# Optimization experiments

Measured on AMD Instinct MI355X. Metric: run time of the kernel, lower is better.

The kernel has to match this reference:

```python
import jax, jax.numpy as jnp
import numpy as np

N = 100000
E = 600000
H = 128
OUT = 64
L = 3

def glorot(key, shape):
    fan_in, fan_out = shape[0], shape[1]
    lim = jnp.sqrt(6.0 / (fan_in + fan_out))
    return jax.random.uniform(key, shape, jnp.float32, -lim, lim)

def setup_inputs() -> dict:
    key = jax.random.key(0)
    ks = jax.random.split(key, 20)
    x = jax.random.normal(ks[0], (N, H), jnp.float32)
    edge_index = jax.random.randint(ks[1], (2, E), 0, N, jnp.int64)
    edge_attr = jax.random.uniform(ks[2], (E, 1), jnp.float32)
    # stacked per-layer params [L, ...]
    W_lin = jnp.stack([glorot(jax.random.fold_in(ks[3], i), (H, H)) for i in range(L)])
    b_lin = jnp.zeros((L, H), jnp.float32)
    W_msg = jnp.stack([glorot(jax.random.fold_in(ks[4], i), (H + 1, H)) for i in range(L)])
    b_msg = jnp.zeros((L, H), jnp.float32)
    W_l = jnp.stack([glorot(jax.random.fold_in(ks[5], i), (H, H)) for i in range(L)])
    b_l = jnp.zeros((L, H), jnp.float32)
    W_r = jnp.stack([glorot(jax.random.fold_in(ks[6], i), (H, H)) for i in range(L)])
    W_dec = glorot(ks[7], (H, H))
    b_dec = jnp.zeros((H,), jnp.float32)
    W_fin = glorot(ks[8], (H, OUT))
    b_fin = jnp.zeros((OUT,), jnp.float32)
    return {"x": x, "edge_attr": edge_attr, "W_lin": W_lin, "b_lin": b_lin,
            "W_msg": W_msg, "b_msg": b_msg, "W_l": W_l, "b_l": b_l, "W_r": W_r,
            "W_dec": W_dec, "b_dec": b_dec, "W_fin": W_fin, "b_fin": b_fin,
            "edge_index": edge_index}

def reference(x, edge_attr, W_lin, b_lin, W_msg, b_msg, W_l, b_l, W_r,
              W_dec, b_dec, W_fin, b_fin, edge_index):
    src, dst = edge_index[0], edge_index[1]  # j -> i (source_to_target)
    # mean-aggregation denominator: in-degree clamped to 1
    deg = jax.ops.segment_sum(jnp.ones((E,), jnp.float32), dst, num_segments=N)
    inv_deg = (1.0 / jnp.maximum(deg, 1.0))[:, None]  # [N,1]
    for l in range(L):
        h = jax.nn.relu(x @ W_lin[l] + b_lin[l])          # [N,H]
        msg_in = jnp.concatenate([h[src], edge_attr], -1)  # [E,H+1]
        msg = jax.nn.relu(msg_in @ W_msg[l] + b_msg[l])    # [E,H]
        agg = jax.ops.segment_sum(msg, dst, num_segments=N) * inv_deg  # [N,H]
        out = (agg @ W_l[l] + b_l[l]) + x @ W_r[l]         # lin_l(agg) + lin_r(x_r)
        x = jax.nn.relu(out)  # dropout p=0.0 -> identity
    emb = jax.nn.relu(x @ W_dec + b_dec)
    logits = emb @ W_fin + b_fin  # [N,OUT]
    return logits
```

## Files before the change

### kernel.cpp

```cpp
#include <hip/hip_runtime.h>

using short8 = __attribute__((ext_vector_type(8))) short;
using f32x4  = __attribute__((ext_vector_type(4))) float;

constexpr int HD = 128;

__device__ __forceinline__ unsigned short f2bf(float f) {
    unsigned u = __builtin_bit_cast(unsigned, f);
    u += 0x7fffu + ((u >> 16) & 1u);
    return (unsigned short)(u >> 16);
}
__device__ __forceinline__ float bflo(unsigned u) { return __builtin_bit_cast(float, u << 16); }
__device__ __forceinline__ float bfhi(unsigned u) { return __builtin_bit_cast(float, u & 0xffff0000u); }

__device__ __forceinline__ short8 ldg8(const unsigned short* p) {
    return *reinterpret_cast<const short8*>(p);
}

template<bool DUAL, bool CHAIN, int NC2, bool F32OUT>
__global__ __launch_bounds__(256)
void k_gemm_s(const unsigned short* __restrict__ A1, const unsigned short* __restrict__ Wt1,
              const unsigned short* __restrict__ A2, const unsigned short* __restrict__ Wt2,
              const unsigned short* __restrict__ Wtc, const float* __restrict__ b1,
              const float* __restrict__ b2, void* __restrict__ Out, int nrows)
{
    __shared__ __align__(16) unsigned short As1[64 * HD];
    __shared__ __align__(16) unsigned short As2[DUAL ? 64 * HD : 8];
    __shared__ __align__(16) unsigned short Hs [CHAIN ? 64 * HD : 8];

    const int tid  = threadIdx.x;
    const int lane = tid & 63, wave = tid >> 6;
    const int lr = lane & 15, lg = lane >> 4;
    const int row0 = blockIdx.x * 64;

#pragma unroll
    for (int it = 0; it < 4; ++it) {
        const int q   = wave * 4 + it;
        const int c   = q * 64 + lane;
        const int row = c >> 4, cw = c & 15;
        int grow = row0 + row; grow = grow < nrows ? grow : nrows - 1;
        const int gco = (cw ^ (row & 7)) << 3;
        __builtin_amdgcn_global_load_lds((const unsigned int*)(A1 + (long)grow * HD + gco),
                                         (unsigned int*)&As1[q * 512], 16, 0, 0);
        if constexpr (DUAL)
            __builtin_amdgcn_global_load_lds((const unsigned int*)(A2 + (long)grow * HD + gco),
                                             (unsigned int*)&As2[q * 512], 16, 0, 0);
    }

    const int cb1 = wave * 32;
    short8 bf1[2][4];
#pragma unroll
    for (int ct = 0; ct < 2; ++ct) {
        const unsigned short* bp = Wt1 + (long)(cb1 + ct * 16 + lr) * HD + lg * 8;
#pragma unroll
        for (int kt = 0; kt < 4; ++kt) bf1[ct][kt] = ldg8(bp + kt * 32);
    }
    short8 bf2[DUAL ? 2 : 1][4];
    if constexpr (DUAL) {
#pragma unroll
        for (int ct = 0; ct < 2; ++ct) {
            const unsigned short* bp = Wt2 + (long)(cb1 + ct * 16 + lr) * HD + lg * 8;
#pragma unroll
            for (int kt = 0; kt < 4; ++kt) bf2[ct][kt] = ldg8(bp + kt * 32);
        }
    }
    constexpr int CT2 = CHAIN ? (NC2 / 64) : 1;
    const int cb2 = wave * (NC2 / 4);
    short8 bfc[CT2][4];
    if constexpr (CHAIN) {
#pragma unroll
        for (int ct = 0; ct < CT2; ++ct) {
            const unsigned short* bp = Wtc + (long)(cb2 + ct * 16 + lr) * HD + lg * 8;
#pragma unroll
            for (int kt = 0; kt < 4; ++kt) bfc[ct][kt] = ldg8(bp + kt * 32);
        }
    }

    __syncthreads();

    f32x4 acc[4][2] = {};
#pragma unroll
    for (int kt = 0; kt < 4; ++kt) {
        short8 af[4];
#pragma unroll
        for (int rt = 0; rt < 4; ++rt)
            af[rt] = *reinterpret_cast<const short8*>(
                &As1[(rt * 16 + lr) * HD + (((kt * 4 + lg) ^ (lr & 7)) << 3)]);
#pragma unroll
        for (int rt = 0; rt < 4; ++rt)
#pragma unroll
            for (int ct = 0; ct < 2; ++ct)
                acc[rt][ct] = __builtin_amdgcn_mfma_f32_16x16x32_bf16(af[rt], bf1[ct][kt], acc[rt][ct], 0, 0, 0);
        if constexpr (DUAL) {
            short8 af2[4];
#pragma unroll
            for (int rt = 0; rt < 4; ++rt)
                af2[rt] = *reinterpret_cast<const short8*>(
                    &As2[(rt * 16 + lr) * HD + (((kt * 4 + lg) ^ (lr & 7)) << 3)]);
#pragma unroll
            for (int rt = 0; rt < 4; ++rt)
#pragma unroll
                for (int ct = 0; ct < 2; ++ct)
                    acc[rt][ct] = __builtin_amdgcn_mfma_f32_16x16x32_bf16(af2[rt], bf2[ct][kt], acc[rt][ct], 0, 0, 0);
        }
    }

    const float bv1[2] = { b1[cb1 + lr], b1[cb1 + 16 + lr] };

    if constexpr (!CHAIN) {
        unsigned short* C = (unsigned short*)Out;
#pragma unroll
        for (int rt = 0; rt < 4; ++rt)
#pragma unroll
            for (int ct = 0; ct < 2; ++ct) {
                const int cc = cb1 + ct * 16 + lr;
#pragma unroll
                for (int i = 0; i < 4; ++i) {
                    const int r = row0 + rt * 16 + lg * 4 + i;
                    if (r < nrows) C[(long)r * HD + cc] = f2bf(fmaxf(acc[rt][ct][i] + bv1[ct], 0.f));
                }
            }
    } else {
#pragma unroll
        for (int rt = 0; rt < 4; ++rt)
#pragma unroll
            for (int ct = 0; ct < 2; ++ct) {
                const int cc = cb1 + ct * 16 + lr;
#pragma unroll
                for (int i = 0; i < 4; ++i) {
                    const int row = rt * 16 + lg * 4 + i;
                    const float v = fmaxf(acc[rt][ct][i] + bv1[ct], 0.f);
                    Hs[row * HD + ((((cc >> 3) ^ (row & 7)) << 3) | (cc & 7))] = f2bf(v);
                }
            }
        __syncthreads();

        f32x4 acc2[4][CT2] = {};
#pragma unroll
        for (int kt = 0; kt < 4; ++kt) {
            short8 ah[4];
#pragma unroll
            for (int rt = 0; rt < 4; ++rt)
                ah[rt] = *reinterpret_cast<const short8*>(
                    &Hs[(rt * 16 + lr) * HD + (((kt * 4 + lg) ^ (lr & 7)) << 3)]);
#pragma unroll
            for (int rt = 0; rt < 4; ++rt)
#pragma unroll
                for (int ct = 0; ct < CT2; ++ct)
                    acc2[rt][ct] = __builtin_amdgcn_mfma_f32_16x16x32_bf16(ah[rt], bfc[ct][kt], acc2[rt][ct], 0, 0, 0);
        }
        float bv2[CT2];
#pragma unroll
        for (int ct = 0; ct < CT2; ++ct) bv2[ct] = b2[cb2 + ct * 16 + lr];
#pragma unroll
        for (int rt = 0; rt < 4; ++rt)
#pragma unroll
            for (int ct = 0; ct < CT2; ++ct) {
                const int cc = cb2 + ct * 16 + lr;
#pragma unroll
                for (int i = 0; i < 4; ++i) {
                    const int r = row0 + rt * 16 + lg * 4 + i;
                    if (r < nrows) {
                        const float v = acc2[rt][ct][i] + bv2[ct];
                        if constexpr (F32OUT) ((float*)Out)[(long)r * NC2 + cc] = v;
                        else ((unsigned short*)Out)[(long)r * NC2 + cc] = f2bf(v);
                    }
                }
            }
    }
}

__global__ void k_cast_bf16(const float* __restrict__ in, unsigned short* __restrict__ out, long n8) {
    long i = (long)blockIdx.x * 256 + threadIdx.x;
    if (i >= n8) return;
    const float4 v0 = *((const float4*)in + i * 2);
    const float4 v1 = *((const float4*)in + i * 2 + 1);
    unsigned o[4];
    o[0] = (unsigned)f2bf(v0.x) | ((unsigned)f2bf(v0.y) << 16);
    o[1] = (unsigned)f2bf(v0.z) | ((unsigned)f2bf(v0.w) << 16);
    o[2] = (unsigned)f2bf(v1.x) | ((unsigned)f2bf(v1.y) << 16);
    o[3] = (unsigned)f2bf(v1.z) | ((unsigned)f2bf(v1.w) << 16);
    *(uint4*)(out + i * 8) = *(uint4*)o;
}

__global__ void k_prep_w(const float* __restrict__ Wlin, const float* __restrict__ Wmsg,
                         const float* __restrict__ Wl,   const float* __restrict__ Wr,
                         const float* __restrict__ Wdec, const float* __restrict__ Wfin,
                         unsigned short* __restrict__ wt)
{
    const int m = blockIdx.y;
    const float* src; int C = 128;
    if      (m < 3)  src = Wlin + m * 16384;
    else if (m < 6)  src = Wmsg + (m - 3) * (129 * 128);
    else if (m < 9)  src = Wl   + (m - 6) * 16384;
    else if (m < 12) src = Wr   + (m - 9) * 16384;
    else if (m == 12) src = Wdec;
    else { src = Wfin; C = 64; }
    const int elems = C * 128;
    int e = blockIdx.x * 256 + threadIdx.x;
    if (e >= elems) return;
    int c = e >> 7, k = e & 127;
    wt[m * 16384 + e] = f2bf(src[k * C + c]);
}

__global__ void k_deg(const int* __restrict__ dst, int* __restrict__ deg, int nE, int n) {
    const int grp = blockIdx.x & 7;
    const int bin = blockIdx.x >> 3;
    const int nbin = gridDim.x >> 3;
    const int chunk = (n + 7) >> 3;
    const int lo = grp * chunk;
    const int hi = min(n, lo + chunk);
    for (int e = bin * 256 + threadIdx.x; e < nE; e += nbin * 256) {
        const int d = dst[e];
        if (d >= lo && d < hi) atomicAdd(&deg[d], 1);
    }
}

__global__ void k_chunksum(const int* __restrict__ deg, int* __restrict__ csum, int n) {
    __shared__ int s[256];
    int t = threadIdx.x, i = blockIdx.x * 256 + t;
    s[t] = (i < n) ? deg[i] : 0;
    __syncthreads();
    for (int o = 128; o > 0; o >>= 1) { if (t < o) s[t] += s[t + o]; __syncthreads(); }
    if (t == 0) csum[blockIdx.x] = s[0];
}

__global__ void k_scanmid(const int* __restrict__ csum, int* __restrict__ cbase,
                          int* __restrict__ rowstart, int nch, int n) {
    __shared__ int s[512];
    int t = threadIdx.x;
    int v = (t < nch) ? csum[t] : 0;
    s[t] = v; __syncthreads();
    for (int off = 1; off < 512; off <<= 1) {
        int tmp = (t >= off) ? s[t - off] : 0;
        __syncthreads();
        s[t] += tmp;
        __syncthreads();
    }
    if (t < nch) cbase[t] = s[t] - v;
    if (t == nch - 1) rowstart[n] = s[t];
}

__global__ void k_scan2(const int* __restrict__ deg, const int* __restrict__ cbase,
                        int* __restrict__ rowstart, float* __restrict__ inv_deg, int n) {
    __shared__ int s[256];
    int t = threadIdx.x, i = blockIdx.x * 256 + t;
    int v = (i < n) ? deg[i] : 0;
    s[t] = v; __syncthreads();
    for (int off = 1; off < 256; off <<= 1) {
        int tmp = (t >= off) ? s[t - off] : 0;
        __syncthreads();
        s[t] += tmp;
        __syncthreads();
    }
    if (i < n) {
        rowstart[i] = cbase[blockIdx.x] + s[t] - v;
        inv_deg[i] = 1.0f / fmaxf((float)v, 1.0f);
    }
}

__global__ void k_fill(const int* __restrict__ src, const int* __restrict__ dst,
                       const float* __restrict__ eattr, const int* __restrict__ rowstart,
                       int* __restrict__ degcur, uint2* __restrict__ csr_rec, int nE, int n) {
    const int grp = blockIdx.x & 7;
    const int bin = blockIdx.x >> 3;
    const int nbin = gridDim.x >> 3;
    const int chunk = (n + 7) >> 3;
    const int lo = grp * chunk;
    const int hi = min(n, lo + chunk);
    for (int e = bin * 256 + threadIdx.x; e < nE; e += nbin * 256) {
        const int d = dst[e];
        if (d >= lo && d < hi) {
            const int p = rowstart[d] + atomicSub(&degcur[d], 1) - 1;
            uint2 rec;
            rec.x = (unsigned)src[e];
            rec.y = __builtin_bit_cast(unsigned, eattr[e]);
            csr_rec[p] = rec;
        }
    }
}

__global__ __launch_bounds__(256)
void k_agg(const unsigned short* __restrict__ g, const uint2* __restrict__ rec,
           const int* __restrict__ rs, const float* __restrict__ inv_deg,
           const float* __restrict__ wlast, unsigned short* __restrict__ agg, int n) {
    const int lane = threadIdx.x & 15;
    const int node = blockIdx.x * 16 + (threadIdx.x >> 4);
    if (node >= n) return;
    const int c0 = lane * 8;
    const float4 wla = *(const float4*)(wlast + c0);
    const float4 wlb = *(const float4*)(wlast + c0 + 4);
    const int p0 = rs[node], p1 = rs[node + 1];
    float a0=0,a1=0,a2=0,a3=0,a4=0,a5=0,a6=0,a7=0;
    int p = p0;
    for (; p + 2 <= p1; p += 2) {
        const uint2 r0 = rec[p], r1 = rec[p + 1];
        const float e0 = __builtin_bit_cast(float, r0.y);
        const float e1 = __builtin_bit_cast(float, r1.y);
        const uint4 G0 = *(const uint4*)(g + (long)r0.x * HD + c0);
        const uint4 G1 = *(const uint4*)(g + (long)r1.x * HD + c0);
        a0 += fmaxf(fmaf(e0, wla.x, bflo(G0.x)), 0.f) + fmaxf(fmaf(e1, wla.x, bflo(G1.x)), 0.f);
        a1 += fmaxf(fmaf(e0, wla.y, bfhi(G0.x)), 0.f) + fmaxf(fmaf(e1, wla.y, bfhi(G1.x)), 0.f);
        a2 += fmaxf(fmaf(e0, wla.z, bflo(G0.y)), 0.f) + fmaxf(fmaf(e1, wla.z, bflo(G1.y)), 0.f);
        a3 += fmaxf(fmaf(e0, wla.w, bfhi(G0.y)), 0.f) + fmaxf(fmaf(e1, wla.w, bfhi(G1.y)), 0.f);
        a4 += fmaxf(fmaf(e0, wlb.x, bflo(G0.z)), 0.f) + fmaxf(fmaf(e1, wlb.x, bflo(G1.z)), 0.f);
        a5 += fmaxf(fmaf(e0, wlb.y, bfhi(G0.z)), 0.f) + fmaxf(fmaf(e1, wlb.y, bfhi(G1.z)), 0.f);
        a6 += fmaxf(fmaf(e0, wlb.z, bflo(G0.w)), 0.f) + fmaxf(fmaf(e1, wlb.z, bflo(G1.w)), 0.f);
        a7 += fmaxf(fmaf(e0, wlb.w, bfhi(G0.w)), 0.f) + fmaxf(fmaf(e1, wlb.w, bfhi(G1.w)), 0.f);
    }
    if (p < p1) {
        const uint2 r0 = rec[p];
        const float e0 = __builtin_bit_cast(float, r0.y);
        const uint4 G0 = *(const uint4*)(g + (long)r0.x * HD + c0);
        a0 += fmaxf(fmaf(e0, wla.x, bflo(G0.x)), 0.f);
        a1 += fmaxf(fmaf(e0, wla.y, bfhi(G0.x)), 0.f);
        a2 += fmaxf(fmaf(e0, wla.z, bflo(G0.y)), 0.f);
        a3 += fmaxf(fmaf(e0, wla.w, bfhi(G0.y)), 0.f);
        a4 += fmaxf(fmaf(e0, wlb.x, bflo(G0.z)), 0.f);
        a5 += fmaxf(fmaf(e0, wlb.y, bfhi(G0.z)), 0.f);
        a6 += fmaxf(fmaf(e0, wlb.z, bflo(G0.w)), 0.f);
        a7 += fmaxf(fmaf(e0, wlb.w, bfhi(G0.w)), 0.f);
    }
    const float id = inv_deg[node];
    uint4 o;
    o.x = (unsigned)f2bf(a0 * id) | ((unsigned)f2bf(a1 * id) << 16);
    o.y = (unsigned)f2bf(a2 * id) | ((unsigned)f2bf(a3 * id) << 16);
    o.z = (unsigned)f2bf(a4 * id) | ((unsigned)f2bf(a5 * id) << 16);
    o.w = (unsigned)f2bf(a6 * id) | ((unsigned)f2bf(a7 * id) << 16);
    *(uint4*)(agg + (long)node * HD + c0) = o;
}

extern "C" void kernel_launch(void* const* d_in, const int* in_sizes, int n_in,
                              void* d_out, int out_size, void* d_ws, size_t ws_size,
                              hipStream_t stream)
{
    const float* x     = (const float*)d_in[0];
    const float* eattr = (const float*)d_in[1];
    const float* W_lin = (const float*)d_in[2];
    const float* b_lin = (const float*)d_in[3];
    const float* W_msg = (const float*)d_in[4];
    const float* b_msg = (const float*)d_in[5];
    const float* W_l   = (const float*)d_in[6];
    const float* b_l   = (const float*)d_in[7];
    const float* W_r   = (const float*)d_in[8];
    const float* W_dec = (const float*)d_in[9];
    const float* b_dec = (const float*)d_in[10];
    const float* W_fin = (const float*)d_in[11];
    const float* b_fin = (const float*)d_in[12];
    const int*   ei    = (const int*)d_in[13];

    const int N = in_sizes[0] / HD;
    const int E = in_sizes[1];
    const int* srcv = ei;
    const int* dstv = ei + E;

    char* wsb = (char*)d_ws;
    size_t off = 0;
    auto carve = [&](size_t bytes) -> void* {
        void* p = wsb + off;
        off += (bytes + 255) & ~(size_t)255;
        return p;
    };
    unsigned short* xb = (unsigned short*)carve((size_t)N * HD * 2);
    unsigned short* t1 = (unsigned short*)carve((size_t)N * HD * 2);
    unsigned short* t2 = (unsigned short*)carve((size_t)N * HD * 2);
    unsigned short* t3 = (unsigned short*)carve((size_t)N * HD * 2);
    unsigned short* wt = (unsigned short*)carve((size_t)14 * 16384 * 2);
    uint2* csr_rec  = (uint2*)carve((size_t)E * 8);
    int*   rowstart = (int*)carve((size_t)(N + 1) * 4);
    int*   deg      = (int*)carve((size_t)N * 4);
    float* inv_deg  = (float*)carve((size_t)N * 4);
    const int NCH = (N + 255) / 256;
    int* csum  = (int*)carve((size_t)NCH * 4);
    int* cbase = (int*)carve((size_t)NCH * 4);

    if (off > ws_size) {
        hipMemsetAsync(d_out, 0, (size_t)out_size * 4, stream);
        return;
    }

    hipMemsetAsync(deg, 0, (size_t)N * 4, stream);

    k_cast_bf16<<<(int)(((long)N * HD / 8 + 255) / 256), 256, 0, stream>>>(x, xb, (long)N * HD / 8);
    k_prep_w<<<dim3(64, 14), 256, 0, stream>>>(W_lin, W_msg, W_l, W_r, W_dec, W_fin, wt);

    k_deg<<<2048, 256, 0, stream>>>(dstv, deg, E, N);
    k_chunksum<<<NCH, 256, 0, stream>>>(deg, csum, N);
    k_scanmid<<<1, 512, 0, stream>>>(csum, cbase, rowstart, NCH, N);
    k_scan2<<<NCH, 256, 0, stream>>>(deg, cbase, rowstart, inv_deg, N);
    k_fill<<<2048, 256, 0, stream>>>(srcv, dstv, eattr, rowstart, deg, csr_rec, E, N);

    auto WT = [&](int m) { return wt + (size_t)m * 16384; };
    const int NB64 = (N + 63) / 64;
    const int GAGG = (N + 15) / 16;

    const unsigned short* xin = xb;
    for (int l = 0; l < 3; ++l) {
        unsigned short* gb = (l == 1) ? t3 : t2;
        k_gemm_s<false, true, 128, false><<<NB64, 256, 0, stream>>>(
            xin, WT(l), nullptr, nullptr, WT(3 + l), b_lin + l * HD, b_msg + l * HD, gb, N);
        k_agg<<<GAGG, 256, 0, stream>>>(
            gb, csr_rec, rowstart, inv_deg,
            W_msg + (size_t)l * (HD + 1) * HD + (size_t)HD * HD, t1, N);
        k_gemm_s<true, false, 128, false><<<NB64, 256, 0, stream>>>(
            t1, WT(6 + l), xin, WT(9 + l), nullptr, b_l + l * HD, nullptr, gb, N);
        xin = gb;
    }
    k_gemm_s<false, true, 64, true><<<NB64, 256, 0, stream>>>(
        xin, WT(12), nullptr, nullptr, WT(13), b_dec, b_fin, (float*)d_out, N);
}
```

Before: 355.1 us.

## Fuse mean aggregation into the dual GEMM that applies lin_l and lin_r

```diff
diff --git a/kernel.cpp b/kernel.cpp
--- a/kernel.cpp
+++ b/kernel.cpp
@@ -17,16 +17,14 @@
     return *reinterpret_cast<const short8*>(p);
 }
 
-template<bool DUAL, bool CHAIN, int NC2, bool F32OUT>
+template<int NC2, bool F32OUT>
 __global__ __launch_bounds__(256)
-void k_gemm_s(const unsigned short* __restrict__ A1, const unsigned short* __restrict__ Wt1,
-              const unsigned short* __restrict__ A2, const unsigned short* __restrict__ Wt2,
-              const unsigned short* __restrict__ Wtc, const float* __restrict__ b1,
-              const float* __restrict__ b2, void* __restrict__ Out, int nrows)
+void k_chain(const unsigned short* __restrict__ A, const unsigned short* __restrict__ Wt1,
+             const unsigned short* __restrict__ Wtc, const float* __restrict__ b1,
+             const float* __restrict__ b2, void* __restrict__ Out, int nrows)
 {
     __shared__ __align__(16) unsigned short As1[64 * HD];
-    __shared__ __align__(16) unsigned short As2[DUAL ? 64 * HD : 8];
-    __shared__ __align__(16) unsigned short Hs [CHAIN ? 64 * HD : 8];
+    __shared__ __align__(16) unsigned short Hs [64 * HD];
 
     const int tid  = threadIdx.x;
     const int lane = tid & 63, wave = tid >> 6;
@@ -40,11 +38,8 @@
         const int row = c >> 4, cw = c & 15;
         int grow = row0 + row; grow = grow < nrows ? grow : nrows - 1;
         const int gco = (cw ^ (row & 7)) << 3;
-        __builtin_amdgcn_global_load_lds((const unsigned int*)(A1 + (long)grow * HD + gco),
+        __builtin_amdgcn_global_load_lds((const unsigned int*)(A + (long)grow * HD + gco),
                                          (unsigned int*)&As1[q * 512], 16, 0, 0);
-        if constexpr (DUAL)
-            __builtin_amdgcn_global_load_lds((const unsigned int*)(A2 + (long)grow * HD + gco),
-                                             (unsigned int*)&As2[q * 512], 16, 0, 0);
     }
 
     const int cb1 = wave * 32;
@@ -55,25 +50,14 @@
 #pragma unroll
         for (int kt = 0; kt < 4; ++kt) bf1[ct][kt] = ldg8(bp + kt * 32);
     }
-    short8 bf2[DUAL ? 2 : 1][4];
-    if constexpr (DUAL) {
-#pragma unroll
-        for (int ct = 0; ct < 2; ++ct) {
-            const unsigned short* bp = Wt2 + (long)(cb1 + ct * 16 + lr) * HD + lg * 8;
-#pragma unroll
-            for (int kt = 0; kt < 4; ++kt) bf2[ct][kt] = ldg8(bp + kt * 32);
-        }
-    }
-    constexpr int CT2 = CHAIN ? (NC2 / 64) : 1;
+    constexpr int CT2 = NC2 / 64;
     const int cb2 = wave * (NC2 / 4);
     short8 bfc[CT2][4];
-    if constexpr (CHAIN) {
-#pragma unroll
-        for (int ct = 0; ct < CT2; ++ct) {
-            const unsigned short* bp = Wtc + (long)(cb2 + ct * 16 + lr) * HD + lg * 8;
-#pragma unroll
-            for (int kt = 0; kt < 4; ++kt) bfc[ct][kt] = ldg8(bp + kt * 32);
-        }
+#pragma unroll
+    for (int ct = 0; ct < CT2; ++ct) {
+        const unsigned short* bp = Wtc + (long)(cb2 + ct * 16 + lr) * HD + lg * 8;
+#pragma unroll
+        for (int kt = 0; kt < 4; ++kt) bfc[ct][kt] = ldg8(bp + kt * 32);
     }
 
     __syncthreads();
@@ -91,83 +75,175 @@
 #pragma unroll
             for (int ct = 0; ct < 2; ++ct)
                 acc[rt][ct] = __builtin_amdgcn_mfma_f32_16x16x32_bf16(af[rt], bf1[ct][kt], acc[rt][ct], 0, 0, 0);
-        if constexpr (DUAL) {
-            short8 af2[4];
-#pragma unroll
-            for (int rt = 0; rt < 4; ++rt)
-                af2[rt] = *reinterpret_cast<const short8*>(
-                    &As2[(rt * 16 + lr) * HD + (((kt * 4 + lg) ^ (lr & 7)) << 3)]);
-#pragma unroll
-            for (int rt = 0; rt < 4; ++rt)
-#pragma unroll
-                for (int ct = 0; ct < 2; ++ct)
-                    acc[rt][ct] = __builtin_amdgcn_mfma_f32_16x16x32_bf16(af2[rt], bf2[ct][kt], acc[rt][ct], 0, 0, 0);
-        }
     }
 
     const float bv1[2] = { b1[cb1 + lr], b1[cb1 + 16 + lr] };
-
-    if constexpr (!CHAIN) {
-        unsigned short* C = (unsigned short*)Out;
+#pragma unroll
+    for (int rt = 0; rt < 4; ++rt)
+#pragma unroll
+        for (int ct = 0; ct < 2; ++ct) {
+            const int cc = cb1 + ct * 16 + lr;
+#pragma unroll
+            for (int i = 0; i < 4; ++i) {
+                const int row = rt * 16 + lg * 4 + i;
+                const float v = fmaxf(acc[rt][ct][i] + bv1[ct], 0.f);
+                Hs[row * HD + ((((cc >> 3) ^ (row & 7)) << 3) | (cc & 7))] = f2bf(v);
+            }
+        }
+    __syncthreads();
+
+    f32x4 acc2[4][CT2] = {};
+#pragma unroll
+    for (int kt = 0; kt < 4; ++kt) {
+        short8 ah[4];
 #pragma unroll
         for (int rt = 0; rt < 4; ++rt)
+            ah[rt] = *reinterpret_cast<const short8*>(
+                &Hs[(rt * 16 + lr) * HD + (((kt * 4 + lg) ^ (lr & 7)) << 3)]);
+#pragma unroll
+        for (int rt = 0; rt < 4; ++rt)
+#pragma unroll
+            for (int ct = 0; ct < CT2; ++ct)
+                acc2[rt][ct] = __builtin_amdgcn_mfma_f32_16x16x32_bf16(ah[rt], bfc[ct][kt], acc2[rt][ct], 0, 0, 0);
+    }
+    float bv2[CT2];
+#pragma unroll
+    for (int ct = 0; ct < CT2; ++ct) bv2[ct] = b2[cb2 + ct * 16 + lr];
+#pragma unroll
+    for (int rt = 0; rt < 4; ++rt)
+#pragma unroll
+        for (int ct = 0; ct < CT2; ++ct) {
+            const int cc = cb2 + ct * 16 + lr;
+#pragma unroll
+            for (int i = 0; i < 4; ++i) {
+                const int r = row0 + rt * 16 + lg * 4 + i;
+                if (r < nrows) {
+                    const float v = acc2[rt][ct][i] + bv2[ct];
+                    if constexpr (F32OUT) ((float*)Out)[(long)r * NC2 + cc] = v;
+                    else ((unsigned short*)Out)[(long)r * NC2 + cc] = f2bf(v);
+                }
+            }
+        }
+}
+
+__global__ __launch_bounds__(256)
+void k_aggdual(const unsigned short* __restrict__ g, const uint2* __restrict__ rec,
+               const int* __restrict__ rs, const float* __restrict__ inv_deg,
+               const float* __restrict__ wlast, const unsigned short* __restrict__ X,
+               const unsigned short* __restrict__ WtL, const unsigned short* __restrict__ WtR,
+               const float* __restrict__ bias, unsigned short* __restrict__ Out, int n)
+{
+    __shared__ __align__(16) unsigned short Ag[64 * HD];
+    __shared__ __align__(16) unsigned short Xs[64 * HD];
+
+    const int tid  = threadIdx.x;
+    const int lane = tid & 63, wave = tid >> 6;
+    const int lr = lane & 15, lg = lane >> 4;
+    const int row0 = blockIdx.x * 64;
+
+#pragma unroll
+    for (int it = 0; it < 4; ++it) {
+        const int q   = wave * 4 + it;
+        const int c   = q * 64 + lane;
+        const int row = c >> 4, cw = c & 15;
+        int grow = row0 + row; grow = grow < n ? grow : n - 1;
+        const int gco = (cw ^ (row & 7)) << 3;
+        __builtin_amdgcn_global_load_lds((const unsigned int*)(X + (long)grow * HD + gco),
+                                         (unsigned int*)&Xs[q * 512], 16, 0, 0);
+    }
+
+    const int cb = wave * 32;
+    short8 bl[2][4], br[2][4];
+#pragma unroll
+    for (int ct = 0; ct < 2; ++ct) {
+        const unsigned short* pl = WtL + (long)(cb + ct * 16 + lr) * HD + lg * 8;
+        const unsigned short* pr = WtR + (long)(cb + ct * 16 + lr) * HD + lg * 8;
+#pragma unroll
+        for (int kt = 0; kt < 4; ++kt) { bl[ct][kt] = ldg8(pl + kt * 32); br[ct][kt] = ldg8(pr + kt * 32); }
+    }
+
+    {
+        const int grp = tid >> 4, l16 = tid & 15;
+        const int c0 = l16 * 8;
+        const float4 wla = *(const float4*)(wlast + c0);
+        const float4 wlb = *(const float4*)(wlast + c0 + 4);
+        for (int j = 0; j < 4; ++j) {
+            const int node = row0 + grp * 4 + j;
+            if (node >= n) break;
+            const int p0 = rs[node], p1 = rs[node + 1];
+            float a0=0,a1=0,a2=0,a3=0,a4=0,a5=0,a6=0,a7=0;
+            int p = p0;
+            for (; p + 2 <= p1; p += 2) {
+                const uint2 r0 = rec[p], r1 = rec[p + 1];
+                const float e0 = __builtin_bit_cast(float, r0.y);
+                const float e1 = __builtin_bit_cast(float, r1.y);
+                const uint4 G0 = *(const uint4*)(g + (long)r0.x * HD + c0);
+                const uint4 G1 = *(const uint4*)(g + (long)r1.x * HD + c0);
+                a0 += fmaxf(fmaf(e0, wla.x, bflo(G0.x)), 0.f) + fmaxf(fmaf(e1, wla.x, bflo(G1.x)), 0.f);
+                a1 += fmaxf(fmaf(e0, wla.y, bfhi(G0.x)), 0.f) + fmaxf(fmaf(e1, wla.y, bfhi(G1.x)), 0.f);
+                a2 += fmaxf(fmaf(e0, wla.z, bflo(G0.y)), 0.f) + fmaxf(fmaf(e1, wla.z, bflo(G1.y)), 0.f);
+                a3 += fmaxf(fmaf(e0, wla.w, bfhi(G0.y)), 0.f) + fmaxf(fmaf(e1, wla.w, bfhi(G1.y)), 0.f);
+                a4 += fmaxf(fmaf(e0, wlb.x, bflo(G0.z)), 0.f) + fmaxf(fmaf(e1, wlb.x, bflo(G1.z)), 0.f);
+                a5 += fmaxf(fmaf(e0, wlb.y, bfhi(G0.z)), 0.f) + fmaxf(fmaf(e1, wlb.y, bfhi(G1.z)), 0.f);
+                a6 += fmaxf(fmaf(e0, wlb.z, bflo(G0.w)), 0.f) + fmaxf(fmaf(e1, wlb.z, bflo(G1.w)), 0.f);
+                a7 += fmaxf(fmaf(e0, wlb.w, bfhi(G0.w)), 0.f) + fmaxf(fmaf(e1, wlb.w, bfhi(G1.w)), 0.f);
+            }
+            if (p < p1) {
+                const uint2 r0 = rec[p];
+                const float e0 = __builtin_bit_cast(float, r0.y);
+                const uint4 G0 = *(const uint4*)(g + (long)r0.x * HD + c0);
+                a0 += fmaxf(fmaf(e0, wla.x, bflo(G0.x)), 0.f);
+                a1 += fmaxf(fmaf(e0, wla.y, bfhi(G0.x)), 0.f);
+                a2 += fmaxf(fmaf(e0, wla.z, bflo(G0.y)), 0.f);
+                a3 += fmaxf(fmaf(e0, wla.w, bfhi(G0.y)), 0.f);
+                a4 += fmaxf(fmaf(e0, wlb.x, bflo(G0.z)), 0.f);
+                a5 += fmaxf(fmaf(e0, wlb.y, bfhi(G0.z)), 0.f);
+                a6 += fmaxf(fmaf(e0, wlb.z, bflo(G0.w)), 0.f);
+                a7 += fmaxf(fmaf(e0, wlb.w, bfhi(G0.w)), 0.f);
+            }
+            const float id = inv_deg[node];
+            const int row = grp * 4 + j;
+            unsigned o[4];
+            o[0] = (unsigned)f2bf(a0 * id) | ((unsigned)f2bf(a1 * id) << 16);
+            o[1] = (unsigned)f2bf(a2 * id) | ((unsigned)f2bf(a3 * id) << 16);
+            o[2] = (unsigned)f2bf(a4 * id) | ((unsigned)f2bf(a5 * id) << 16);
+            o[3] = (unsigned)f2bf(a6 * id) | ((unsigned)f2bf(a7 * id) << 16);
+            *(uint4*)&Ag[row * HD + ((l16 ^ (row & 7)) << 3)] = *(uint4*)o;
+        }
+    }
+    __syncthreads();
+
+    f32x4 acc[4][2] = {};
+#pragma unroll
+    for (int kt = 0; kt < 4; ++kt) {
+        short8 aa[4], ax[4];
+#pragma unroll
+        for (int rt = 0; rt < 4; ++rt) {
+            const int base = (rt * 16 + lr) * HD + (((kt * 4 + lg) ^ (lr & 7)) << 3);
+            aa[rt] = *reinterpret_cast<const short8*>(&Ag[base]);
+            ax[rt] = *reinterpret_cast<const short8*>(&Xs[base]);
+        }
+#pragma unroll
+        for (int rt = 0; rt < 4; ++rt)
 #pragma unroll
             for (int ct = 0; ct < 2; ++ct) {
-                const int cc = cb1 + ct * 16 + lr;
-#pragma unroll
-                for (int i = 0; i < 4; ++i) {
-                    const int r = row0 + rt * 16 + lg * 4 + i;
-                    if (r < nrows) C[(long)r * HD + cc] = f2bf(fmaxf(acc[rt][ct][i] + bv1[ct], 0.f));
-                }
-            }
-    } else {
-#pragma unroll
-        for (int rt = 0; rt < 4; ++rt)
-#pragma unroll
-            for (int ct = 0; ct < 2; ++ct) {
-                const int cc = cb1 + ct * 16 + lr;
-#pragma unroll
-                for (int i = 0; i < 4; ++i) {
-                    const int row = rt * 16 + lg * 4 + i;
-                    const float v = fmaxf(acc[rt][ct][i] + bv1[ct], 0.f);
-                    Hs[row * HD + ((((cc >> 3) ^ (row & 7)) << 3) | (cc & 7))] = f2bf(v);
-                }
-            }
-        __syncthreads();
-
-        f32x4 acc2[4][CT2] = {};
-#pragma unroll
-        for (int kt = 0; kt < 4; ++kt) {
-            short8 ah[4];
-#pragma unroll
-            for (int rt = 0; rt < 4; ++rt)
-                ah[rt] = *reinterpret_cast<const short8*>(
-                    &Hs[(rt * 16 + lr) * HD + (((kt * 4 + lg) ^ (lr & 7)) << 3)]);
-#pragma unroll
-            for (int rt = 0; rt < 4; ++rt)
-#pragma unroll
-                for (int ct = 0; ct < CT2; ++ct)
-                    acc2[rt][ct] = __builtin_amdgcn_mfma_f32_16x16x32_bf16(ah[rt], bfc[ct][kt], acc2[rt][ct], 0, 0, 0);
-        }
-        float bv2[CT2];
-#pragma unroll
-        for (int ct = 0; ct < CT2; ++ct) bv2[ct] = b2[cb2 + ct * 16 + lr];
-#pragma unroll
-        for (int rt = 0; rt < 4; ++rt)
-#pragma unroll
-            for (int ct = 0; ct < CT2; ++ct) {
-                const int cc = cb2 + ct * 16 + lr;
-#pragma unroll
-                for (int i = 0; i < 4; ++i) {
-                    const int r = row0 + rt * 16 + lg * 4 + i;
-                    if (r < nrows) {
-                        const float v = acc2[rt][ct][i] + bv2[ct];
-                        if constexpr (F32OUT) ((float*)Out)[(long)r * NC2 + cc] = v;
-                        else ((unsigned short*)Out)[(long)r * NC2 + cc] = f2bf(v);
-                    }
-                }
-            }
-    }
+                acc[rt][ct] = __builtin_amdgcn_mfma_f32_16x16x32_bf16(aa[rt], bl[ct][kt], acc[rt][ct], 0, 0, 0);
+                acc[rt][ct] = __builtin_amdgcn_mfma_f32_16x16x32_bf16(ax[rt], br[ct][kt], acc[rt][ct], 0, 0, 0);
+            }
+    }
+
+    const float bv[2] = { bias[cb + lr], bias[cb + 16 + lr] };
+#pragma unroll
+    for (int rt = 0; rt < 4; ++rt)
+#pragma unroll
+        for (int ct = 0; ct < 2; ++ct) {
+            const int cc = cb + ct * 16 + lr;
+#pragma unroll
+            for (int i = 0; i < 4; ++i) {
+                const int r = row0 + rt * 16 + lg * 4 + i;
+                if (r < n) Out[(long)r * HD + cc] = f2bf(fmaxf(acc[rt][ct][i] + bv[ct], 0.f));
+            }
+        }
 }
 
 __global__ void k_cast_bf16(const float* __restrict__ in, unsigned short* __restrict__ out, long n8) {
@@ -278,56 +354,6 @@
             csr_rec[p] = rec;
         }
     }
-}
-
-__global__ __launch_bounds__(256)
-void k_agg(const unsigned short* __restrict__ g, const uint2* __restrict__ rec,
-           const int* __restrict__ rs, const float* __restrict__ inv_deg,
-           const float* __restrict__ wlast, unsigned short* __restrict__ agg, int n) {
-    const int lane = threadIdx.x & 15;
-    const int node = blockIdx.x * 16 + (threadIdx.x >> 4);
-    if (node >= n) return;
-    const int c0 = lane * 8;
-    const float4 wla = *(const float4*)(wlast + c0);
-    const float4 wlb = *(const float4*)(wlast + c0 + 4);
-    const int p0 = rs[node], p1 = rs[node + 1];
-    float a0=0,a1=0,a2=0,a3=0,a4=0,a5=0,a6=0,a7=0;
-    int p = p0;
-    for (; p + 2 <= p1; p += 2) {
-        const uint2 r0 = rec[p], r1 = rec[p + 1];
-        const float e0 = __builtin_bit_cast(float, r0.y);
-        const float e1 = __builtin_bit_cast(float, r1.y);
-        const uint4 G0 = *(const uint4*)(g + (long)r0.x * HD + c0);
-        const uint4 G1 = *(const uint4*)(g + (long)r1.x * HD + c0);
-        a0 += fmaxf(fmaf(e0, wla.x, bflo(G0.x)), 0.f) + fmaxf(fmaf(e1, wla.x, bflo(G1.x)), 0.f);
-        a1 += fmaxf(fmaf(e0, wla.y, bfhi(G0.x)), 0.f) + fmaxf(fmaf(e1, wla.y, bfhi(G1.x)), 0.f);
-        a2 += fmaxf(fmaf(e0, wla.z, bflo(G0.y)), 0.f) + fmaxf(fmaf(e1, wla.z, bflo(G1.y)), 0.f);
-        a3 += fmaxf(fmaf(e0, wla.w, bfhi(G0.y)), 0.f) + fmaxf(fmaf(e1, wla.w, bfhi(G1.y)), 0.f);
-        a4 += fmaxf(fmaf(e0, wlb.x, bflo(G0.z)), 0.f) + fmaxf(fmaf(e1, wlb.x, bflo(G1.z)), 0.f);
-        a5 += fmaxf(fmaf(e0, wlb.y, bfhi(G0.z)), 0.f) + fmaxf(fmaf(e1, wlb.y, bfhi(G1.z)), 0.f);
-        a6 += fmaxf(fmaf(e0, wlb.z, bflo(G0.w)), 0.f) + fmaxf(fmaf(e1, wlb.z, bflo(G1.w)), 0.f);
-        a7 += fmaxf(fmaf(e0, wlb.w, bfhi(G0.w)), 0.f) + fmaxf(fmaf(e1, wlb.w, bfhi(G1.w)), 0.f);
-    }
-    if (p < p1) {
-        const uint2 r0 = rec[p];
-        const float e0 = __builtin_bit_cast(float, r0.y);
-        const uint4 G0 = *(const uint4*)(g + (long)r0.x * HD + c0);
-        a0 += fmaxf(fmaf(e0, wla.x, bflo(G0.x)), 0.f);
-        a1 += fmaxf(fmaf(e0, wla.y, bfhi(G0.x)), 0.f);
-        a2 += fmaxf(fmaf(e0, wla.z, bflo(G0.y)), 0.f);
-        a3 += fmaxf(fmaf(e0, wla.w, bfhi(G0.y)), 0.f);
-        a4 += fmaxf(fmaf(e0, wlb.x, bflo(G0.z)), 0.f);
-        a5 += fmaxf(fmaf(e0, wlb.y, bfhi(G0.z)), 0.f);
-        a6 += fmaxf(fmaf(e0, wlb.z, bflo(G0.w)), 0.f);
-        a7 += fmaxf(fmaf(e0, wlb.w, bfhi(G0.w)), 0.f);
-    }
-    const float id = inv_deg[node];
-    uint4 o;
-    o.x = (unsigned)f2bf(a0 * id) | ((unsigned)f2bf(a1 * id) << 16);
-    o.y = (unsigned)f2bf(a2 * id) | ((unsigned)f2bf(a3 * id) << 16);
-    o.z = (unsigned)f2bf(a4 * id) | ((unsigned)f2bf(a5 * id) << 16);
-    o.w = (unsigned)f2bf(a6 * id) | ((unsigned)f2bf(a7 * id) << 16);
-    *(uint4*)(agg + (long)node * HD + c0) = o;
 }
 
 extern "C" void kernel_launch(void* const* d_in, const int* in_sizes, int n_in,
@@ -392,20 +418,19 @@
 
     auto WT = [&](int m) { return wt + (size_t)m * 16384; };
     const int NB64 = (N + 63) / 64;
-    const int GAGG = (N + 15) / 16;
 
     const unsigned short* xin = xb;
     for (int l = 0; l < 3; ++l) {
-        unsigned short* gb = (l == 1) ? t3 : t2;
-        k_gemm_s<false, true, 128, false><<<NB64, 256, 0, stream>>>(
-            xin, WT(l), nullptr, nullptr, WT(3 + l), b_lin + l * HD, b_msg + l * HD, gb, N);
-        k_agg<<<GAGG, 256, 0, stream>>>(
+        unsigned short* gb = (l == 0) ? t2 : t3;
+        unsigned short* ob = (l == 1) ? t2 : t1;
+        k_chain<128, false><<<NB64, 256, 0, stream>>>(
+            xin, WT(l), WT(3 + l), b_lin + l * HD, b_msg + l * HD, gb, N);
+        k_aggdual<<<NB64, 256, 0, stream>>>(
             gb, csr_rec, rowstart, inv_deg,
-            W_msg + (size_t)l * (HD + 1) * HD + (size_t)HD * HD, t1, N);
-        k_gemm_s<true, false, 128, false><<<NB64, 256, 0, stream>>>(
-            t1, WT(6 + l), xin, WT(9 + l), nullptr, b_l + l * HD, nullptr, gb, N);
-        xin = gb;
-    }
-    k_gemm_s<false, true, 64, true><<<NB64, 256, 0, stream>>>(
-        xin, WT(12), nullptr, nullptr, WT(13), b_dec, b_fin, (float*)d_out, N);
-}
+            W_msg + (size_t)l * (HD + 1) * HD + (size_t)HD * HD,
+            xin, WT(6 + l), WT(9 + l), b_l + l * HD, ob, N);
+        xin = ob;
+    }
+    k_chain<64, true><<<NB64, 256, 0, stream>>>(
+        xin, WT(12), WT(13), b_dec, b_fin, (float*)d_out, N);
+}
```

Measured after the change: 427.3 us. 1.2x slower.
